# Kernel tuning notes

Measured on AMD Instinct MI355X. Metric: run time of the kernel, lower is better.

## Reference

```python
import jax, jax.numpy as jnp
import numpy as np

N = 50000      # nodes
E = 800000     # edges (before self-loops)
DIN = 256
HID = 64
HEADS = 4
DOUT = 128
NEG_SLOPE = 0.2  # PyG GATConv default leaky-relu slope


def setup_inputs() -> dict:
    key = jax.random.key(0)
    ks = jax.random.split(key, 10)
    s = 0.05
    x = jax.random.normal(ks[0], (N, DIN), jnp.float32)
    edge_index = jax.random.randint(ks[1], (2, E), 0, N, dtype=jnp.int32)
    W1 = jax.random.normal(ks[2], (DIN, HEADS * HID), jnp.float32) * s
    a1_src = jax.random.normal(ks[3], (HEADS, HID), jnp.float32) * s
    a1_dst = jax.random.normal(ks[4], (HEADS, HID), jnp.float32) * s
    b1 = jnp.zeros((HEADS * HID,), jnp.float32)
    W2 = jax.random.normal(ks[5], (HEADS * HID, DOUT), jnp.float32) * s
    a2_src = jax.random.normal(ks[6], (1, DOUT), jnp.float32) * s
    a2_dst = jax.random.normal(ks[7], (1, DOUT), jnp.float32) * s
    b2 = jnp.zeros((DOUT,), jnp.float32)
    return {"x": x, "edge_index": edge_index,
            "W1": W1, "a1_src": a1_src, "a1_dst": a1_dst, "b1": b1,
            "W2": W2, "a2_src": a2_src, "a2_dst": a2_dst, "b2": b2}


def _gat_conv(x, src, dst, W, a_src, a_dst, b, heads, concat):
    """PyG-style GATConv (self-loops already appended to src/dst)."""
    n = x.shape[0]
    h = (x @ W).reshape(n, heads, -1)               # [N, H, C]
    e_src = jnp.einsum('nhc,hc->nh', h, a_src)       # [N, H]
    e_dst = jnp.einsum('nhc,hc->nh', h, a_dst)
    logits = jax.nn.leaky_relu(e_src[src] + e_dst[dst], NEG_SLOPE)  # [E', H]
    # segment softmax over incoming edges of each dst node
    m = jax.ops.segment_max(logits, dst, num_segments=n)
    ex = jnp.exp(logits - m[dst])
    denom = jax.ops.segment_sum(ex, dst, num_segments=n)
    alpha = ex / (denom[dst] + 1e-16)                # [E', H]
    msg = alpha[:, :, None] * h[src]                 # [E', H, C]
    out = jax.ops.segment_sum(msg, dst, num_segments=n)  # [N, H, C]
    if concat:
        out = out.reshape(n, -1)
    else:
        out = out.mean(axis=1)
    return out + b


def reference(x, edge_index, W1, a1_src, a1_dst, b1, W2, a2_src, a2_dst, b2):
    n = x.shape[0]
    loop = jnp.arange(n, dtype=edge_index.dtype)
    src = jnp.concatenate([edge_index[0], loop])
    dst = jnp.concatenate([edge_index[1], loop])
    h = jax.nn.elu(_gat_conv(x, src, dst, W1, a1_src, a1_dst, b1, HEADS, True))
    h = jax.nn.elu(_gat_conv(h, src, dst, W2, a2_src, a2_dst, b2, 1, False))
    return h.mean(axis=1)  # [N]
```

## Files before the change

kernel.cpp:

```cpp
#include <hip/hip_runtime.h>
#include <math.h>

#define N_NODES 50000
#define M_PAD   50048
#define N_EDGES 800000
#define EP (N_EDGES + N_NODES)
#define DIN 256
#define HEADS 4
#define HID 64
#define F1 256
#define F2 128
#define NEG_SLOPE 0.2f
#define SCAN_NBLK ((N_NODES + 255)/256)

typedef short bf16x8 __attribute__((ext_vector_type(8)));
typedef float f32x4  __attribute__((ext_vector_type(4)));

static __device__ __forceinline__ float leaky(float x){ return x > 0.f ? x : NEG_SLOPE*x; }
static __device__ __forceinline__ float elu_f(float x){ return x > 0.f ? x : (__expf(x)-1.f); }
static __device__ __forceinline__ float b2f(unsigned short u){ return __uint_as_float(((unsigned)u)<<16); }
static __device__ __forceinline__ unsigned short f2b(float f){
  unsigned u = __float_as_uint(f);
  return (unsigned short)((u + 0x7fffu + ((u>>16)&1u)) >> 16);
}

__global__ __launch_bounds__(256) void k_hist(const int* __restrict__ dst, int* __restrict__ counts){
  int e = blockIdx.x*256 + threadIdx.x;
  if (e >= EP) return;
  int d = (e < N_EDGES) ? dst[e] : (e - N_EDGES);
  atomicAdd(&counts[d], 1);
}

__global__ __launch_bounds__(256) void k_scan1(const int* __restrict__ counts,
                                               int* __restrict__ exc, int* __restrict__ bsum){
  int i = blockIdx.x*256 + threadIdx.x;
  int v = (i < N_NODES) ? counts[i] : 0;
  int lane = threadIdx.x & 63, wave = threadIdx.x >> 6;
  int inc = v;
  #pragma unroll
  for (int off=1; off<64; off<<=1){
    int n = __shfl_up(inc, off);
    if (lane >= off) inc += n;
  }
  __shared__ int wsum[4];
  if (lane == 63) wsum[wave] = inc;
  __syncthreads();
  int wpre = 0;
  #pragma unroll
  for (int w=0; w<4; w++) if (w < wave) wpre += wsum[w];
  if (i < N_NODES) exc[i] = wpre + inc - v;
  if (threadIdx.x == 255) bsum[blockIdx.x] = wpre + inc;
}

__global__ __launch_bounds__(256) void k_scan2(const int* __restrict__ bsum,
                                               int* __restrict__ bpref, int* __restrict__ offsets){
  int i = threadIdx.x;
  int v = (i < SCAN_NBLK) ? bsum[i] : 0;
  int lane = threadIdx.x & 63, wave = threadIdx.x >> 6;
  int inc = v;
  #pragma unroll
  for (int off=1; off<64; off<<=1){
    int n = __shfl_up(inc, off);
    if (lane >= off) inc += n;
  }
  __shared__ int wsum[4];
  if (lane == 63) wsum[wave] = inc;
  __syncthreads();
  int wpre = 0;
  #pragma unroll
  for (int w=0; w<4; w++) if (w < wave) wpre += wsum[w];
  if (i < SCAN_NBLK) bpref[i] = wpre + inc - v;
  if (i == 255) offsets[N_NODES] = wpre + inc;
}

__global__ __launch_bounds__(256) void k_scan3d(const int* __restrict__ exc, const int* __restrict__ bpref,
                                                int* __restrict__ offsets, int* __restrict__ cursor,
                                                const int* __restrict__ counts,
                                                int* __restrict__ dbin, int* __restrict__ bcount){
  __shared__ int h[256];
  h[threadIdx.x] = 0;
  __syncthreads();
  int i = blockIdx.x*256 + threadIdx.x;
  if (i < N_NODES){
    int o = exc[i] + bpref[blockIdx.x];
    offsets[i] = o;
    cursor[i] = o;
    int b = counts[i]; if (b > 255) b = 255;
    atomicAdd(&h[b], 1);
  }
  __syncthreads();
  int c = h[threadIdx.x];
  bcount[(size_t)blockIdx.x*256 + threadIdx.x] = c;
  if (c) atomicAdd(&dbin[threadIdx.x], c);
}

__global__ __launch_bounds__(256) void k_scatter(const int* __restrict__ src, const int* __restrict__ dst,
                          int* __restrict__ cursor, int* __restrict__ sorted_src, int* __restrict__ sorted_dst){
  int e = blockIdx.x*256 + threadIdx.x;
  if (e >= EP) return;
  int s, d;
  if (e < N_EDGES){ s = src[e]; d = dst[e]; } else { s = d = e - N_EDGES; }
  int pos = atomicAdd(&cursor[d], 1);
  sorted_src[pos] = s;
  sorted_dst[pos] = d;
}

__global__ __launch_bounds__(256) void k_dscan_col(const int* __restrict__ dbin, const int* __restrict__ bcount,
                                                   int* __restrict__ colbase){
  int i = threadIdx.x;
  int v = dbin[i];
  int lane = threadIdx.x & 63, wave = threadIdx.x >> 6;
  int inc = v;
  #pragma unroll
  for (int off=1; off<64; off<<=1){
    int n = __shfl_up(inc, off);
    if (lane >= off) inc += n;
  }
  __shared__ int wsum[4];
  if (lane == 63) wsum[wave] = inc;
  __syncthreads();
  int wpre = 0;
  #pragma unroll
  for (int w=0; w<4; w++) if (w < wave) wpre += wsum[w];
  int run = wpre + inc - v;
  for (int blk=0; blk<SCAN_NBLK; blk++){
    colbase[(size_t)blk*256 + i] = run;
    run += bcount[(size_t)blk*256 + i];
  }
}

__global__ __launch_bounds__(256) void k_dscatter(const int* __restrict__ counts, const int* __restrict__ colbase,
                                                  int* __restrict__ perm){
  __shared__ int h[256];
  h[threadIdx.x] = 0;
  __syncthreads();
  int i = blockIdx.x*256 + threadIdx.x;
  if (i < N_NODES){
    int b = counts[i]; if (b > 255) b = 255;
    int r = atomicAdd(&h[b], 1);
    perm[colbase[(size_t)blockIdx.x*256 + b] + r] = i;
  }
}

__global__ __launch_bounds__(256) void k_splitA(const float* __restrict__ X,
                         unsigned short* __restrict__ Ahi){
  int gid = blockIdx.x*256 + threadIdx.x;
  size_t base = (size_t)gid*4;
  int row = (int)(base >> 8);
  ushort4 hi;
  if (row < N_NODES){
    float4 v = *(const float4*)(X + base);
    hi.x=f2b(v.x); hi.y=f2b(v.y); hi.z=f2b(v.z); hi.w=f2b(v.w);
  } else {
    hi = {0,0,0,0};
  }
  *(ushort4*)(Ahi + base) = hi;
}

__global__ __launch_bounds__(256) void k_splitWT2(const float* __restrict__ W1, const float* __restrict__ W2,
                          unsigned short* __restrict__ Bt1, unsigned short* __restrict__ Bt2){
  int t = blockIdx.x*256 + threadIdx.x;
  if (t < DIN*F1){
    int n = t / DIN, k = t % DIN;
    Bt1[(unsigned)n*DIN + k] = f2b(W1[(unsigned)k*F1 + n]);
  } else if (t < DIN*F1 + F1*F2){
    int u = t - DIN*F1;
    int n = u / F1, k = u % F1;
    Bt2[(unsigned)n*F1 + k] = f2b(W2[(unsigned)k*F2 + n]);
  }
}

__global__ __launch_bounds__(256) void k_gemm1f(
    const unsigned short* __restrict__ A, const unsigned short* __restrict__ Bt,
    const float* __restrict__ a1s, const float* __restrict__ a1d,
    unsigned short* __restrict__ Cbf, float* __restrict__ es, float* __restrict__ ed){
  const int K = 256, Nc = F1;
  int tid = threadIdx.x;
  int wave = tid>>6, lane = tid&63;
  int wc = wave;
  int row0 = blockIdx.x*32;
  int col0 = wc*64;
  int lrow = lane&15, lk = (lane>>4)*8;
  f32x4 acc[2][4] = {};
  bf16x8 aA[2], bA[4], aB[2], bB[4];
  auto LOADF = [&](bf16x8* av, bf16x8* bv, int KS){
    #pragma unroll
    for (int i=0;i<2;i++)
      av[i] = *(const bf16x8*)(A  + (unsigned)(row0 + i*16 + lrow)*K + KS + lk);
    #pragma unroll
    for (int j=0;j<4;j++)
      bv[j] = *(const bf16x8*)(Bt + (unsigned)(col0 + j*16 + lrow)*K + KS + lk);
  };
  auto MFMAS = [&](bf16x8* av, bf16x8* bv){
    #pragma unroll
    for (int i=0;i<2;i++)
      #pragma unroll
      for (int j=0;j<4;j++)
        acc[i][j] = __builtin_amdgcn_mfma_f32_16x16x32_bf16(av[i], bv[j], acc[i][j], 0,0,0);
  };
  LOADF(aA,bA,0);
  #pragma unroll
  for (int ks=0; ks<K; ks+=64){
    LOADF(aB,bB,ks+32);
    MFMAS(aA,bA);
    if (ks+64 < K) LOADF(aA,bA,ks+64);
    MFMAS(aB,bB);
  }
  int crow = (lane>>4)*4, ccol = lane&15;
  #pragma unroll
  for (int i=0;i<2;i++)
    #pragma unroll
    for (int j=0;j<4;j++)
      #pragma unroll
      for (int q=0;q<4;q++){
        int r = row0 + i*16 + crow + q;
        int c = col0 + j*16 + ccol;
        Cbf[(unsigned)r*Nc + c] = f2b(acc[i][j][q]);
      }
  float avs[4], avd[4];
  #pragma unroll
  for (int j=0;j<4;j++){
    avs[j] = a1s[wc*64 + j*16 + ccol];
    avd[j] = a1d[wc*64 + j*16 + ccol];
  }
  #pragma unroll
  for (int i=0;i<2;i++){
    #pragma unroll
    for (int q=0;q<4;q++){
      float ps = acc[i][0][q]*avs[0] + acc[i][1][q]*avs[1] + acc[i][2][q]*avs[2] + acc[i][3][q]*avs[3];
      float pd = acc[i][0][q]*avd[0] + acc[i][1][q]*avd[1] + acc[i][2][q]*avd[2] + acc[i][3][q]*avd[3];
      #pragma unroll
      for (int off=1; off<16; off<<=1){ ps += __shfl_xor(ps,off); pd += __shfl_xor(pd,off); }
      if ((lane&15)==0){
        int r = row0 + i*16 + crow + q;
        es[(unsigned)r*4 + wc] = ps;
        ed[(unsigned)r*4 + wc] = pd;
      }
    }
  }
}

__global__ __launch_bounds__(256) void k_gemm2(
    const unsigned short* __restrict__ A, const unsigned short* __restrict__ Bt,
    unsigned short* __restrict__ Cbf){
  const int K = 256, Nc = F2;
  int tid = threadIdx.x;
  int wave = tid>>6, lane = tid&63;
  int wr = wave>>1, wc = wave&1;
  int row0 = blockIdx.x*64 + wr*32;
  int col0 = wc*64;
  int lrow = lane&15, lk = (lane>>4)*8;
  f32x4 acc[2][4] = {};
  bf16x8 aA[2], bA[4], aB[2], bB[4];
  auto LOADF = [&](bf16x8* av, bf16x8* bv, int KS){
    #pragma unroll
    for (int i=0;i<2;i++)
      av[i] = *(const bf16x8*)(A  + (unsigned)(row0 + i*16 + lrow)*K + KS + lk);
    #pragma unroll
    for (int j=0;j<4;j++)
      bv[j] = *(const bf16x8*)(Bt + (unsigned)(col0 + j*16 + lrow)*K + KS + lk);
  };
  auto MFMAS = [&](bf16x8* av, bf16x8* bv){
    #pragma unroll
    for (int i=0;i<2;i++)
      #pragma unroll
      for (int j=0;j<4;j++)
        acc[i][j] = __builtin_amdgcn_mfma_f32_16x16x32_bf16(av[i], bv[j], acc[i][j], 0,0,0);
  };
  LOADF(aA,bA,0);
  #pragma unroll
  for (int ks=0; ks<K; ks+=64){
    LOADF(aB,bB,ks+32);
    MFMAS(aA,bA);
    if (ks+64 < K) LOADF(aA,bA,ks+64);
    MFMAS(aB,bB);
  }
  int crow = (lane>>4)*4, ccol = lane&15;
  #pragma unroll
  for (int i=0;i<2;i++)
    #pragma unroll
    for (int j=0;j<4;j++)
      #pragma unroll
      for (int q=0;q<4;q++){
        int r = row0 + i*16 + crow + q;
        int c = col0 + j*16 + ccol;
        Cbf[(unsigned)r*Nc + c] = f2b(acc[i][j][q]);
      }
}

__global__ __launch_bounds__(256) void k_edot2(const unsigned short* __restrict__ h2bf, const float* __restrict__ a_src,
                        const float* __restrict__ a_dst, float* __restrict__ es, float* __restrict__ ed){
  int wave=threadIdx.x>>6, lane=threadIdx.x&63;
  int n = blockIdx.x*4+wave; if (n>=N_NODES) return;
  ushort2 hv = ((const ushort2*)(h2bf + (unsigned)n*F2))[lane];
  float2 s2 = ((const float2*)a_src)[lane];
  float2 d2 = ((const float2*)a_dst)[lane];
  float h0=b2f(hv.x), h1=b2f(hv.y);
  float ps = h0*s2.x + h1*s2.y;
  float pd = h0*d2.x + h1*d2.y;
  #pragma unroll
  for (int m=1;m<64;m<<=1){ ps += __shfl_xor(ps,m); pd += __shfl_xor(pd,m); }
  if (lane==0){ es[n]=ps; ed[n]=pd; }
}

__global__ __launch_bounds__(256) void k_eexp1(const int* __restrict__ ssrc, const int* __restrict__ sdst,
                        const float* __restrict__ es, const float* __restrict__ ed,
                        float* __restrict__ ex){
  int e = blockIdx.x*256 + threadIdx.x;
  if (e >= EP) return;
  unsigned s = (unsigned)ssrc[e], d = (unsigned)sdst[e];
  float4 ev = *(const float4*)(es + s*4);
  float4 dv = *(const float4*)(ed + d*4);
  float4 o;
  o.x = __expf(leaky(ev.x+dv.x));
  o.y = __expf(leaky(ev.y+dv.y));
  o.z = __expf(leaky(ev.z+dv.z));
  o.w = __expf(leaky(ev.w+dv.w));
  *(float4*)(ex + (unsigned)e*4) = o;
}

__global__ __launch_bounds__(256) void k_eexp2(const int* __restrict__ ssrc, const int* __restrict__ sdst,
                        const float* __restrict__ es, const float* __restrict__ ed,
                        float* __restrict__ ex){
  int e = blockIdx.x*256 + threadIdx.x;
  if (e >= EP) return;
  unsigned s = (unsigned)ssrc[e], d = (unsigned)sdst[e];
  ex[e] = __expf(leaky(es[s] + ed[d]));
}

__global__ __launch_bounds__(256) void k_agg1(const unsigned short* __restrict__ h1bf, const float* __restrict__ ex1,
                       const int* __restrict__ offsets,
                       const int* __restrict__ ssrc, const int* __restrict__ perm,
                       const float* __restrict__ b1,
                       unsigned short* __restrict__ A2hi){
  int wave = threadIdx.x>>6, lane = threadIdx.x&63;
  int idx = blockIdx.x*4 + wave;
  if (idx >= M_PAD) return;
  if (idx >= N_NODES){
    ushort4 z = {0,0,0,0};
    ((ushort4*)(A2hi + (unsigned)idx*F1))[lane] = z;
    return;
  }
  int d = perm[idx];
  unsigned beg = (unsigned)offsets[d], end = (unsigned)offsets[d+1];
  unsigned deg = end - beg;
  unsigned head = (unsigned)(lane>>4);
  const ushort4* __restrict__ hb = (const ushort4*)h1bf;
  const float* __restrict__ exh = ex1 + head;
  float s0=0.f,s1=0.f,s2=0.f,s3=0.f;
  float4 acc0={0,0,0,0}, acc1={0,0,0,0}, acc2={0,0,0,0}, acc3={0,0,0,0};
  unsigned j=0;
  for (; j+4<=deg; j+=4){
    unsigned e0=beg+j;
    unsigned sn0=(unsigned)ssrc[e0], sn1=(unsigned)ssrc[e0+1], sn2=(unsigned)ssrc[e0+2], sn3=(unsigned)ssrc[e0+3];
    float x0 = exh[e0*4], x1 = exh[e0*4+4], x2 = exh[e0*4+8], x3 = exh[e0*4+12];
    ushort4 v0 = hb[sn0*64 + lane];
    ushort4 v1 = hb[sn1*64 + lane];
    ushort4 v2 = hb[sn2*64 + lane];
    ushort4 v3 = hb[sn3*64 + lane];
    s0+=x0; s1+=x1; s2+=x2; s3+=x3;
    acc0.x=fmaf(x0,b2f(v0.x),acc0.x); acc0.y=fmaf(x0,b2f(v0.y),acc0.y); acc0.z=fmaf(x0,b2f(v0.z),acc0.z); acc0.w=fmaf(x0,b2f(v0.w),acc0.w);
    acc1.x=fmaf(x1,b2f(v1.x),acc1.x); acc1.y=fmaf(x1,b2f(v1.y),acc1.y); acc1.z=fmaf(x1,b2f(v1.z),acc1.z); acc1.w=fmaf(x1,b2f(v1.w),acc1.w);
    acc2.x=fmaf(x2,b2f(v2.x),acc2.x); acc2.y=fmaf(x2,b2f(v2.y),acc2.y); acc2.z=fmaf(x2,b2f(v2.z),acc2.z); acc2.w=fmaf(x2,b2f(v2.w),acc2.w);
    acc3.x=fmaf(x3,b2f(v3.x),acc3.x); acc3.y=fmaf(x3,b2f(v3.y),acc3.y); acc3.z=fmaf(x3,b2f(v3.z),acc3.z); acc3.w=fmaf(x3,b2f(v3.w),acc3.w);
  }
  for (; j<deg; j++){
    unsigned e0=beg+j;
    unsigned sn=(unsigned)ssrc[e0];
    float x = exh[e0*4];
    ushort4 v = hb[sn*64 + lane];
    s0 += x;
    acc0.x=fmaf(x,b2f(v.x),acc0.x); acc0.y=fmaf(x,b2f(v.y),acc0.y);
    acc0.z=fmaf(x,b2f(v.z),acc0.z); acc0.w=fmaf(x,b2f(v.w),acc0.w);
  }
  float inv = 1.f/(s0+s1+s2+s3+1e-16f);
  float4 acc;
  acc.x = (acc0.x+acc1.x+acc2.x+acc3.x)*inv;
  acc.y = (acc0.y+acc1.y+acc2.y+acc3.y)*inv;
  acc.z = (acc0.z+acc1.z+acc2.z+acc3.z)*inv;
  acc.w = (acc0.w+acc1.w+acc2.w+acc3.w)*inv;
  float4 bb = *(const float4*)(b1 + lane*4);
  ushort4 hi;
  hi.x = f2b(elu_f(acc.x + bb.x));
  hi.y = f2b(elu_f(acc.y + bb.y));
  hi.z = f2b(elu_f(acc.z + bb.z));
  hi.w = f2b(elu_f(acc.w + bb.w));
  ((ushort4*)(A2hi + (unsigned)d*F1))[lane] = hi;
}

__global__ __launch_bounds__(256) void k_agg2(const unsigned short* __restrict__ h2bf, const float* __restrict__ ex2,
                       const int* __restrict__ offsets,
                       const int* __restrict__ ssrc, const int* __restrict__ perm,
                       const float* __restrict__ b2, float* __restrict__ out){
  int wave=threadIdx.x>>6, lane=threadIdx.x&63;
  int idx = blockIdx.x*4+wave; if (idx>=N_NODES) return;
  int d = perm[idx];
  unsigned beg=(unsigned)offsets[d], end=(unsigned)offsets[d+1];
  unsigned deg=end-beg;
  const ushort2* __restrict__ hb = (const ushort2*)h2bf;
  float s0=0.f,s1=0.f,s2=0.f,s3=0.f;
  float2 acc0={0,0}, acc1={0,0}, acc2={0,0}, acc3={0,0};
  unsigned j=0;
  for (; j+4<=deg; j+=4){
    unsigned e0=beg+j;
    unsigned sn0=(unsigned)ssrc[e0], sn1=(unsigned)ssrc[e0+1], sn2=(unsigned)ssrc[e0+2], sn3=(unsigned)ssrc[e0+3];
    float x0=ex2[e0], x1=ex2[e0+1], x2=ex2[e0+2], x3=ex2[e0+3];
    ushort2 v0 = hb[sn0*64 + lane];
    ushort2 v1 = hb[sn1*64 + lane];
    ushort2 v2 = hb[sn2*64 + lane];
    ushort2 v3 = hb[sn3*64 + lane];
    s0+=x0; s1+=x1; s2+=x2; s3+=x3;
    acc0.x=fmaf(x0,b2f(v0.x),acc0.x); acc0.y=fmaf(x0,b2f(v0.y),acc0.y);
    acc1.x=fmaf(x1,b2f(v1.x),acc1.x); acc1.y=fmaf(x1,b2f(v1.y),acc1.y);
    acc2.x=fmaf(x2,b2f(v2.x),acc2.x); acc2.y=fmaf(x2,b2f(v2.y),acc2.y);
    acc3.x=fmaf(x3,b2f(v3.x),acc3.x); acc3.y=fmaf(x3,b2f(v3.y),acc3.y);
  }
  for (; j<deg; j++){
    unsigned e0=beg+j;
    unsigned sn=(unsigned)ssrc[e0];
    float x = ex2[e0];
    ushort2 v = hb[sn*64 + lane];
    s0 += x;
    acc0.x=fmaf(x,b2f(v.x),acc0.x); acc0.y=fmaf(x,b2f(v.y),acc0.y);
  }
  float inv = 1.f/(s0+s1+s2+s3+1e-16f);
  float2 acc;
  acc.x = (acc0.x+acc1.x+acc2.x+acc3.x)*inv;
  acc.y = (acc0.y+acc1.y+acc2.y+acc3.y)*inv;
  float2 bb = *(const float2*)(b2 + lane*2);
  float r = elu_f(acc.x+bb.x) + elu_f(acc.y+bb.y);
  #pragma unroll
  for (int off=1;off<64;off<<=1) r += __shfl_xor(r,off);
  if (lane==0) out[d] = r * (1.f/128.f);
}

extern "C" void kernel_launch(void* const* d_in, const int* in_sizes, int n_in,
                              void* d_out, int out_size, void* d_ws, size_t ws_size,
                              hipStream_t stream) {
  const float* x   = (const float*)d_in[0];
  const int*   ei  = (const int*)d_in[1];
  const int*   esrc = ei;
  const int*   edst = ei + N_EDGES;
  const float* W1  = (const float*)d_in[2];
  const float* a1s = (const float*)d_in[3];
  const float* a1d = (const float*)d_in[4];
  const float* b1  = (const float*)d_in[5];
  const float* W2  = (const float*)d_in[6];
  const float* a2s = (const float*)d_in[7];
  const float* a2d = (const float*)d_in[8];
  const float* b2  = (const float*)d_in[9];
  float* out = (float*)d_out;

  char* ws = (char*)d_ws;
  size_t off = 0;
  auto alloc = [&](size_t bytes)->void*{ void* p = ws + off; off += (bytes + 255) & ~(size_t)255; return p; };
  unsigned short* A1hi = (unsigned short*)alloc((size_t)M_PAD*F1*2);
  unsigned short* h1bf = (unsigned short*)alloc((size_t)M_PAD*F1*2);
  unsigned short* h2bf = (unsigned short*)alloc((size_t)M_PAD*F2*2);
  unsigned short* Bt1hi= (unsigned short*)alloc((size_t)F1*DIN*2);
  unsigned short* Bt2hi= (unsigned short*)alloc((size_t)F2*F1*2);
  float* e1s   = (float*)alloc((size_t)M_PAD*HEADS*4);
  float* e1d   = (float*)alloc((size_t)M_PAD*HEADS*4);
  float* e2s   = (float*)alloc((size_t)N_NODES*4);
  float* e2d   = (float*)alloc((size_t)N_NODES*4);
  float* ex1   = (float*)alloc((size_t)EP*HEADS*4);
  float* ex2   = (float*)alloc((size_t)EP*4);
  int*   counts= (int*)alloc((size_t)N_NODES*4);
  int*   offs  = (int*)alloc((size_t)(N_NODES+1)*4);
  int*   cursor= (int*)alloc((size_t)N_NODES*4);
  int*   exc   = (int*)alloc((size_t)N_NODES*4);
  int*   bsum  = (int*)alloc((size_t)SCAN_NBLK*4);
  int*   bpref = (int*)alloc((size_t)SCAN_NBLK*4);
  int*   perm  = (int*)alloc((size_t)N_NODES*4);
  int*   dbin  = (int*)alloc((size_t)256*4);
  int*   bcount= (int*)alloc((size_t)SCAN_NBLK*256*4);
  int*   colbase=(int*)alloc((size_t)SCAN_NBLK*256*4);
  int*   ssrc  = (int*)alloc((size_t)EP*4);
  int*   sdst  = (int*)alloc((size_t)EP*4);
  unsigned short* A2hi = A1hi;

  hipMemsetAsync(counts, 0, (size_t)N_NODES*4, stream);
  hipMemsetAsync(dbin, 0, (size_t)256*4, stream);
  k_hist<<<(EP+255)/256, 256, 0, stream>>>(edst, counts);
  k_scan1<<<SCAN_NBLK, 256, 0, stream>>>(counts, exc, bsum);
  k_scan2<<<1, 256, 0, stream>>>(bsum, bpref, offs);
  k_scan3d<<<SCAN_NBLK, 256, 0, stream>>>(exc, bpref, offs, cursor, counts, dbin, bcount);
  k_scatter<<<(EP+255)/256, 256, 0, stream>>>(esrc, edst, cursor, ssrc, sdst);
  k_dscan_col<<<1, 256, 0, stream>>>(dbin, bcount, colbase);
  k_dscatter<<<SCAN_NBLK, 256, 0, stream>>>(counts, colbase, perm);

  k_splitA<<<(M_PAD*F1/4 + 255)/256, 256, 0, stream>>>(x, A1hi);
  k_splitWT2<<<(DIN*F1 + F1*F2 + 255)/256, 256, 0, stream>>>(W1, W2, Bt1hi, Bt2hi);

  k_gemm1f<<<M_PAD/32, 256, 0, stream>>>(A1hi, Bt1hi, a1s, a1d, h1bf, e1s, e1d);
  k_eexp1<<<(EP+255)/256, 256, 0, stream>>>(ssrc, sdst, e1s, e1d, ex1);
  k_agg1<<<(M_PAD+3)/4, 256, 0, stream>>>(h1bf, ex1, offs, ssrc, perm, b1, A2hi);

  k_gemm2<<<M_PAD/64, 256, 0, stream>>>(A2hi, Bt2hi, h2bf);
  k_edot2<<<(N_NODES+3)/4, 256, 0, stream>>>(h2bf, a2s, a2d, e2s, e2d);
  k_eexp2<<<(EP+255)/256, 256, 0, stream>>>(ssrc, sdst, e2s, e2d, ex2);
  k_agg2<<<(N_NODES+3)/4, 256, 0, stream>>>(h2bf, ex2, offs, ssrc, perm, b2, out);
}
```

Before: 328.5 us.

## Fuse preprocessing launches, fold block-prefix scan, and enlarge GEMM row tiles

Merges the histogram, input bf16 conversion and weight-transpose kernels into one launch split by block ranges. Drops the single-block scan2 kernel: each scan3d block now sums the preceding block totals itself. The degree-column scan runs as an extra block of the edge scatter kernel. Separately, both GEMMs compute twice as many rows per block (4x4 MFMA tiles per wave), which cuts launch count and serialized tiny kernels but raises register pressure and lowers block count.

```diff
diff --git a/kernel.cpp b/kernel.cpp
--- a/kernel.cpp
+++ b/kernel.cpp
@@ -12,6 +12,10 @@
 #define F2 128
 #define NEG_SLOPE 0.2f
 #define SCAN_NBLK ((N_NODES + 255)/256)
+#define HIST_NB ((EP + 255)/256)
+#define SA_NB (M_PAD*F1/4/256)
+#define WT_TOT (DIN*F1 + F1*F2)
+#define WT_NB ((WT_TOT + 255)/256)
 
 typedef short bf16x8 __attribute__((ext_vector_type(8)));
 typedef float f32x4  __attribute__((ext_vector_type(4)));
@@ -24,11 +28,40 @@
   return (unsigned short)((u + 0x7fffu + ((u>>16)&1u)) >> 16);
 }
 
-__global__ __launch_bounds__(256) void k_hist(const int* __restrict__ dst, int* __restrict__ counts){
-  int e = blockIdx.x*256 + threadIdx.x;
-  if (e >= EP) return;
-  int d = (e < N_EDGES) ? dst[e] : (e - N_EDGES);
-  atomicAdd(&counts[d], 1);
+__global__ __launch_bounds__(256) void k_prep(const float* __restrict__ X, unsigned short* __restrict__ Ahi,
+    const float* __restrict__ W1, const float* __restrict__ W2,
+    unsigned short* __restrict__ Bt1, unsigned short* __restrict__ Bt2,
+    const int* __restrict__ dst, int* __restrict__ counts){
+  unsigned b = blockIdx.x;
+  if (b < SA_NB){
+    int gid = b*256 + threadIdx.x;
+    size_t base = (size_t)gid*4;
+    int row = (int)(base >> 8);
+    ushort4 hi;
+    if (row < N_NODES){
+      float4 v = *(const float4*)(X + base);
+      hi.x=f2b(v.x); hi.y=f2b(v.y); hi.z=f2b(v.z); hi.w=f2b(v.w);
+    } else {
+      hi = {0,0,0,0};
+    }
+    *(ushort4*)(Ahi + base) = hi;
+  } else if (b < SA_NB + WT_NB){
+    int t = (b - SA_NB)*256 + threadIdx.x;
+    if (t < DIN*F1){
+      int n = t / DIN, k = t % DIN;
+      Bt1[(unsigned)n*DIN + k] = f2b(W1[(unsigned)k*F1 + n]);
+    } else if (t < WT_TOT){
+      int u = t - DIN*F1;
+      int n = u / F1, k = u % F1;
+      Bt2[(unsigned)n*F1 + k] = f2b(W2[(unsigned)k*F2 + n]);
+    }
+  } else {
+    int e = (b - SA_NB - WT_NB)*256 + threadIdx.x;
+    if (e < EP){
+      int d = (e < N_EDGES) ? dst[e] : (e - N_EDGES);
+      atomicAdd(&counts[d], 1);
+    }
+  }
 }
 
 __global__ __launch_bounds__(256) void k_scan1(const int* __restrict__ counts,
@@ -52,80 +85,68 @@
   if (threadIdx.x == 255) bsum[blockIdx.x] = wpre + inc;
 }
 
-__global__ __launch_bounds__(256) void k_scan2(const int* __restrict__ bsum,
-                                               int* __restrict__ bpref, int* __restrict__ offsets){
-  int i = threadIdx.x;
-  int v = (i < SCAN_NBLK) ? bsum[i] : 0;
-  int lane = threadIdx.x & 63, wave = threadIdx.x >> 6;
-  int inc = v;
-  #pragma unroll
-  for (int off=1; off<64; off<<=1){
-    int n = __shfl_up(inc, off);
-    if (lane >= off) inc += n;
-  }
-  __shared__ int wsum[4];
-  if (lane == 63) wsum[wave] = inc;
+__global__ __launch_bounds__(256) void k_scan3d(const int* __restrict__ exc, const int* __restrict__ bsum,
+                                                const int* __restrict__ counts,
+                                                int* __restrict__ offsets, int* __restrict__ cursor,
+                                                int* __restrict__ dbin, int* __restrict__ bcount){
+  int t = threadIdx.x;
+  int lane = t & 63, wave = t >> 6;
+  int v = (t < (int)blockIdx.x) ? bsum[t] : 0;
+  #pragma unroll
+  for (int off=1; off<64; off<<=1) v += __shfl_xor(v, off);
+  __shared__ int ws[4];
+  __shared__ int hh[256];
+  if (lane == 0) ws[wave] = v;
+  hh[t] = 0;
   __syncthreads();
-  int wpre = 0;
-  #pragma unroll
-  for (int w=0; w<4; w++) if (w < wave) wpre += wsum[w];
-  if (i < SCAN_NBLK) bpref[i] = wpre + inc - v;
-  if (i == 255) offsets[N_NODES] = wpre + inc;
-}
-
-__global__ __launch_bounds__(256) void k_scan3d(const int* __restrict__ exc, const int* __restrict__ bpref,
-                                                int* __restrict__ offsets, int* __restrict__ cursor,
-                                                const int* __restrict__ counts,
-                                                int* __restrict__ dbin, int* __restrict__ bcount){
-  __shared__ int h[256];
-  h[threadIdx.x] = 0;
-  __syncthreads();
-  int i = blockIdx.x*256 + threadIdx.x;
+  int bpref = ws[0] + ws[1] + ws[2] + ws[3];
+  int i = blockIdx.x*256 + t;
   if (i < N_NODES){
-    int o = exc[i] + bpref[blockIdx.x];
+    int o = exc[i] + bpref;
     offsets[i] = o;
     cursor[i] = o;
     int b = counts[i]; if (b > 255) b = 255;
-    atomicAdd(&h[b], 1);
-  }
+    atomicAdd(&hh[b], 1);
+  }
+  if (i == 0) offsets[N_NODES] = EP;
   __syncthreads();
-  int c = h[threadIdx.x];
-  bcount[(size_t)blockIdx.x*256 + threadIdx.x] = c;
-  if (c) atomicAdd(&dbin[threadIdx.x], c);
-}
-
-__global__ __launch_bounds__(256) void k_scatter(const int* __restrict__ src, const int* __restrict__ dst,
-                          int* __restrict__ cursor, int* __restrict__ sorted_src, int* __restrict__ sorted_dst){
-  int e = blockIdx.x*256 + threadIdx.x;
-  if (e >= EP) return;
-  int s, d;
-  if (e < N_EDGES){ s = src[e]; d = dst[e]; } else { s = d = e - N_EDGES; }
-  int pos = atomicAdd(&cursor[d], 1);
-  sorted_src[pos] = s;
-  sorted_dst[pos] = d;
-}
-
-__global__ __launch_bounds__(256) void k_dscan_col(const int* __restrict__ dbin, const int* __restrict__ bcount,
-                                                   int* __restrict__ colbase){
-  int i = threadIdx.x;
-  int v = dbin[i];
-  int lane = threadIdx.x & 63, wave = threadIdx.x >> 6;
-  int inc = v;
-  #pragma unroll
-  for (int off=1; off<64; off<<=1){
-    int n = __shfl_up(inc, off);
-    if (lane >= off) inc += n;
-  }
-  __shared__ int wsum[4];
-  if (lane == 63) wsum[wave] = inc;
-  __syncthreads();
-  int wpre = 0;
-  #pragma unroll
-  for (int w=0; w<4; w++) if (w < wave) wpre += wsum[w];
-  int run = wpre + inc - v;
-  for (int blk=0; blk<SCAN_NBLK; blk++){
-    colbase[(size_t)blk*256 + i] = run;
-    run += bcount[(size_t)blk*256 + i];
+  int c = hh[t];
+  bcount[(unsigned)blockIdx.x*256 + t] = c;
+  if (c) atomicAdd(&dbin[t], c);
+}
+
+__global__ __launch_bounds__(256) void k_scatter_dcol(const int* __restrict__ src, const int* __restrict__ dst,
+                          int* __restrict__ cursor, int* __restrict__ sorted_src, int* __restrict__ sorted_dst,
+                          const int* __restrict__ dbin, const int* __restrict__ bcount, int* __restrict__ colbase){
+  if (blockIdx.x < HIST_NB){
+    int e = blockIdx.x*256 + threadIdx.x;
+    if (e >= EP) return;
+    int s, d;
+    if (e < N_EDGES){ s = src[e]; d = dst[e]; } else { s = d = e - N_EDGES; }
+    int pos = atomicAdd(&cursor[d], 1);
+    sorted_src[pos] = s;
+    sorted_dst[pos] = d;
+  } else {
+    int i = threadIdx.x;
+    int v = dbin[i];
+    int lane = i & 63, wave = i >> 6;
+    int inc = v;
+    #pragma unroll
+    for (int off=1; off<64; off<<=1){
+      int n = __shfl_up(inc, off);
+      if (lane >= off) inc += n;
+    }
+    __shared__ int wsum[4];
+    if (lane == 63) wsum[wave] = inc;
+    __syncthreads();
+    int wpre = 0;
+    #pragma unroll
+    for (int w=0; w<4; w++) if (w < wave) wpre += wsum[w];
+    int run = wpre + inc - v;
+    for (int blk=0; blk<SCAN_NBLK; blk++){
+      colbase[(unsigned)blk*256 + i] = run;
+      run += bcount[(unsigned)blk*256 + i];
+    }
   }
 }
 
@@ -138,35 +159,7 @@
   if (i < N_NODES){
     int b = counts[i]; if (b > 255) b = 255;
     int r = atomicAdd(&h[b], 1);
-    perm[colbase[(size_t)blockIdx.x*256 + b] + r] = i;
-  }
-}
-
-__global__ __launch_bounds__(256) void k_splitA(const float* __restrict__ X,
-                         unsigned short* __restrict__ Ahi){
-  int gid = blockIdx.x*256 + threadIdx.x;
-  size_t base = (size_t)gid*4;
-  int row = (int)(base >> 8);
-  ushort4 hi;
-  if (row < N_NODES){
-    float4 v = *(const float4*)(X + base);
-    hi.x=f2b(v.x); hi.y=f2b(v.y); hi.z=f2b(v.z); hi.w=f2b(v.w);
-  } else {
-    hi = {0,0,0,0};
-  }
-  *(ushort4*)(Ahi + base) = hi;
-}
-
-__global__ __launch_bounds__(256) void k_splitWT2(const float* __restrict__ W1, const float* __restrict__ W2,
-                          unsigned short* __restrict__ Bt1, unsigned short* __restrict__ Bt2){
-  int t = blockIdx.x*256 + threadIdx.x;
-  if (t < DIN*F1){
-    int n = t / DIN, k = t % DIN;
-    Bt1[(unsigned)n*DIN + k] = f2b(W1[(unsigned)k*F1 + n]);
-  } else if (t < DIN*F1 + F1*F2){
-    int u = t - DIN*F1;
-    int n = u / F1, k = u % F1;
-    Bt2[(unsigned)n*F1 + k] = f2b(W2[(unsigned)k*F2 + n]);
+    perm[colbase[(unsigned)blockIdx.x*256 + b] + r] = i;
   }
 }
 
@@ -178,22 +171,21 @@
   int tid = threadIdx.x;
   int wave = tid>>6, lane = tid&63;
   int wc = wave;
-  int row0 = blockIdx.x*32;
+  int row0 = blockIdx.x*64;
   int col0 = wc*64;
   int lrow = lane&15, lk = (lane>>4)*8;
-  f32x4 acc[2][4] = {};
-  bf16x8 aA[2], bA[4], aB[2], bB[4];
+  f32x4 acc[4][4] = {};
+  bf16x8 aA[4], bA[4], aB[4], bB[4];
   auto LOADF = [&](bf16x8* av, bf16x8* bv, int KS){
     #pragma unroll
-    for (int i=0;i<2;i++)
+    for (int i=0;i<4;i++){
       av[i] = *(const bf16x8*)(A  + (unsigned)(row0 + i*16 + lrow)*K + KS + lk);
-    #pragma unroll
-    for (int j=0;j<4;j++)
-      bv[j] = *(const bf16x8*)(Bt + (unsigned)(col0 + j*16 + lrow)*K + KS + lk);
+      bv[i] = *(const bf16x8*)(Bt + (unsigned)(col0 + i*16 + lrow)*K + KS + lk);
+    }
   };
   auto MFMAS = [&](bf16x8* av, bf16x8* bv){
     #pragma unroll
-    for (int i=0;i<2;i++)
+    for (int i=0;i<4;i++)
       #pragma unroll
       for (int j=0;j<4;j++)
         acc[i][j] = __builtin_amdgcn_mfma_f32_16x16x32_bf16(av[i], bv[j], acc[i][j], 0,0,0);
@@ -208,7 +200,7 @@
   }
   int crow = (lane>>4)*4, ccol = lane&15;
   #pragma unroll
-  for (int i=0;i<2;i++)
+  for (int i=0;i<4;i++)
     #pragma unroll
     for (int j=0;j<4;j++)
       #pragma unroll
@@ -224,7 +216,7 @@
     avd[j] = a1d[wc*64 + j*16 + ccol];
   }
   #pragma unroll
-  for (int i=0;i<2;i++){
+  for (int i=0;i<4;i++){
     #pragma unroll
     for (int q=0;q<4;q++){
       float ps = acc[i][0][q]*avs[0] + acc[i][1][q]*avs[1] + acc[i][2][q]*avs[2] + acc[i][3][q]*avs[3];
@@ -247,22 +239,21 @@
   int tid = threadIdx.x;
   int wave = tid>>6, lane = tid&63;
   int wr = wave>>1, wc = wave&1;
-  int row0 = blockIdx.x*64 + wr*32;
+  int row0 = blockIdx.x*128 + wr*64;
   int col0 = wc*64;
   int lrow = lane&15, lk = (lane>>4)*8;
-  f32x4 acc[2][4] = {};
-  bf16x8 aA[2], bA[4], aB[2], bB[4];
+  f32x4 acc[4][4] = {};
+  bf16x8 aA[4], bA[4], aB[4], bB[4];
   auto LOADF = [&](bf16x8* av, bf16x8* bv, int KS){
     #pragma unroll
-    for (int i=0;i<2;i++)
+    for (int i=0;i<4;i++){
       av[i] = *(const bf16x8*)(A  + (unsigned)(row0 + i*16 + lrow)*K + KS + lk);
-    #pragma unroll
-    for (int j=0;j<4;j++)
-      bv[j] = *(const bf16x8*)(Bt + (unsigned)(col0 + j*16 + lrow)*K + KS + lk);
+      bv[i] = *(const bf16x8*)(Bt + (unsigned)(col0 + i*16 + lrow)*K + KS + lk);
+    }
   };
   auto MFMAS = [&](bf16x8* av, bf16x8* bv){
     #pragma unroll
-    for (int i=0;i<2;i++)
+    for (int i=0;i<4;i++)
       #pragma unroll
       for (int j=0;j<4;j++)
         acc[i][j] = __builtin_amdgcn_mfma_f32_16x16x32_bf16(av[i], bv[j], acc[i][j], 0,0,0);
@@ -277,7 +268,7 @@
   }
   int crow = (lane>>4)*4, ccol = lane&15;
   #pragma unroll
-  for (int i=0;i<2;i++)
+  for (int i=0;i<4;i++)
     #pragma unroll
     for (int j=0;j<4;j++)
       #pragma unroll
@@ -470,7 +461,6 @@
   int*   cursor= (int*)alloc((size_t)N_NODES*4);
   int*   exc   = (int*)alloc((size_t)N_NODES*4);
   int*   bsum  = (int*)alloc((size_t)SCAN_NBLK*4);
-  int*   bpref = (int*)alloc((size_t)SCAN_NBLK*4);
   int*   perm  = (int*)alloc((size_t)N_NODES*4);
   int*   dbin  = (int*)alloc((size_t)256*4);
   int*   bcount= (int*)alloc((size_t)SCAN_NBLK*256*4);
@@ -481,23 +471,18 @@
 
   hipMemsetAsync(counts, 0, (size_t)N_NODES*4, stream);
   hipMemsetAsync(dbin, 0, (size_t)256*4, stream);
-  k_hist<<<(EP+255)/256, 256, 0, stream>>>(edst, counts);
+  k_prep<<<SA_NB + WT_NB + HIST_NB, 256, 0, stream>>>(x, A1hi, W1, W2, Bt1hi, Bt2hi, edst, counts);
   k_scan1<<<SCAN_NBLK, 256, 0, stream>>>(counts, exc, bsum);
-  k_scan2<<<1, 256, 0, stream>>>(bsum, bpref, offs);
-  k_scan3d<<<SCAN_NBLK, 256, 0, stream>>>(exc, bpref, offs, cursor, counts, dbin, bcount);
-  k_scatter<<<(EP+255)/256, 256, 0, stream>>>(esrc, edst, cursor, ssrc, sdst);
-  k_dscan_col<<<1, 256, 0, stream>>>(dbin, bcount, colbase);
+  k_scan3d<<<SCAN_NBLK, 256, 0, stream>>>(exc, bsum, counts, offs, cursor, dbin, bcount);
+  k_scatter_dcol<<<HIST_NB + 1, 256, 0, stream>>>(esrc, edst, cursor, ssrc, sdst, dbin, bcount, colbase);
   k_dscatter<<<SCAN_NBLK, 256, 0, stream>>>(counts, colbase, perm);
 
-  k_splitA<<<(M_PAD*F1/4 + 255)/256, 256, 0, stream>>>(x, A1hi);
-  k_splitWT2<<<(DIN*F1 + F1*F2 + 255)/256, 256, 0, stream>>>(W1, W2, Bt1hi, Bt2hi);
-
-  k_gemm1f<<<M_PAD/32, 256, 0, stream>>>(A1hi, Bt1hi, a1s, a1d, h1bf, e1s, e1d);
-  k_eexp1<<<(EP+255)/256, 256, 0, stream>>>(ssrc, sdst, e1s, e1d, ex1);
+  k_gemm1f<<<M_PAD/64, 256, 0, stream>>>(A1hi, Bt1hi, a1s, a1d, h1bf, e1s, e1d);
+  k_eexp1<<<HIST_NB, 256, 0, stream>>>(ssrc, sdst, e1s, e1d, ex1);
   k_agg1<<<(M_PAD+3)/4, 256, 0, stream>>>(h1bf, ex1, offs, ssrc, perm, b1, A2hi);
 
-  k_gemm2<<<M_PAD/64, 256, 0, stream>>>(A2hi, Bt2hi, h2bf);
+  k_gemm2<<<M_PAD/128, 256, 0, stream>>>(A2hi, Bt2hi, h2bf);
   k_edot2<<<(N_NODES+3)/4, 256, 0, stream>>>(h2bf, a2s, a2d, e2s, e2d);
-  k_eexp2<<<(EP+255)/256, 256, 0, stream>>>(ssrc, sdst, e2s, e2d, ex2);
+  k_eexp2<<<HIST_NB, 256, 0, stream>>>(ssrc, sdst, e2s, e2d, ex2);
   k_agg2<<<(N_NODES+3)/4, 256, 0, stream>>>(h2bf, ex2, offs, ssrc, perm, b2, out);
 }
```

Result: faster. 308.6 us (-6.1%).
